# Kernel tuning notes

Hardware: AMD Instinct MI355X
Metric: run time of the kernel (lower is better)

The kernel has to match this reference:

```python
import jax, jax.numpy as jnp
import numpy as np

EMB = 32  # DGM_c.input_dim

def setup_inputs() -> dict:
    key = jax.random.key(0)
    k1, k2, k3 = jax.random.split(key, 3)
    G, n, F = 32, 1024, 128
    N = G * n
    x = jax.random.normal(k1, (N, F), dtype=jnp.float32)
    W = jax.random.normal(k2, (F, EMB), dtype=jnp.float32) / np.sqrt(F)
    temperature = jnp.float32(1.0)   # nn.Parameter init 1.0
    threshold = jnp.float32(0.5)     # nn.Parameter init 0.5
    batch = jnp.repeat(jnp.arange(G, dtype=jnp.int32), n)  # equal-sized graphs
    edge_index = jax.random.randint(k3, (2, 262144), 0, N, dtype=jnp.int32)
    return {"x": x, "W": W, "temperature": temperature, "threshold": threshold,
            "batch": batch, "edge_index": edge_index, "num_graphs": G}


def reference(x, W, temperature, threshold, batch, edge_index, num_graphs):
    # x: [N, F]; equal-sized graphs of n nodes each (batch is sorted, contiguous)
    N = x.shape[0]
    G = num_graphs
    n = N // G

    # embed_f: linear projection to EMB dims (edge structure unused by this embed_f)
    xe = x @ W                                  # [N, EMB]

    # scale<0 branch fires only for the FIRST graph; centroid/scale are detached
    x0 = xe[:n]                                 # graph 0 embedding
    centroid = jax.lax.stop_gradient(jnp.mean(x0, axis=0))             # [EMB]
    scale = jax.lax.stop_gradient(0.9 / jnp.max(jnp.abs(x0 - centroid)))

    xg = ((xe - centroid) * scale).reshape(G, n, EMB)

    # squared pairwise euclidean distances per graph (cdist**2, clamped >= 0)
    sq = jnp.sum(xg * xg, axis=-1)              # [G, n]
    D = jnp.maximum(sq[:, :, None] + sq[:, None, :]
                    - 2.0 * jnp.einsum('gnd,gmd->gnm', xg, xg), 0.0)   # [G, n, n]

    A = jax.nn.sigmoid(temperature * (jnp.abs(threshold) - D))         # [G, n, n]

    # sigmoid > 0 everywhere => dense_to_sparse keeps every entry, row-major,
    # with per-graph node offsets added back.
    edge_weight = A.reshape(-1)                 # [G*n*n]
    ii = jnp.arange(n, dtype=jnp.int32)
    gi = jnp.broadcast_to(ii[:, None], (n, n)).reshape(-1)  # row index
    gj = jnp.broadcast_to(ii[None, :], (n, n)).reshape(-1)  # col index
    off = (jnp.arange(G, dtype=jnp.int32) * n)[:, None]     # [G, 1]
    src = (off + gi[None, :]).reshape(-1)
    dst = (off + gj[None, :]).reshape(-1)
    edge_index_out = jnp.stack([src, dst])      # [2, G*n*n]

    return xe, edge_index_out, edge_weight
```

## Files before the change

### kernel.cpp

```cpp
#include <hip/hip_runtime.h>

#define FDIM 128
#define EMB 32

__global__ __launch_bounds__(256) void k_gemm(const float* __restrict__ x,
                                              const float* __restrict__ Wm,
                                              float* __restrict__ xe) {
    __shared__ float sW[FDIM * EMB];
    const int t = threadIdx.x;
#pragma unroll
    for (int i = 0; i < (FDIM * EMB) / (256 * 4); ++i) {
        int idx = (t + i * 256) * 4;
        *(float4*)(sW + idx) = *(const float4*)(Wm + idx);
    }
    __syncthreads();

    const int r0 = blockIdx.x * 128 + (t >> 3) * 4;
    const int e0 = (t & 7) * 4;

    float acc[4][4];
#pragma unroll
    for (int i = 0; i < 4; ++i)
#pragma unroll
        for (int j = 0; j < 4; ++j) acc[i][j] = 0.f;

    for (int k = 0; k < FDIM; k += 4) {
        float4 w0 = *(const float4*)(sW + (k + 0) * EMB + e0);
        float4 w1 = *(const float4*)(sW + (k + 1) * EMB + e0);
        float4 w2 = *(const float4*)(sW + (k + 2) * EMB + e0);
        float4 w3 = *(const float4*)(sW + (k + 3) * EMB + e0);
#pragma unroll
        for (int rr = 0; rr < 4; ++rr) {
            float4 xq = *(const float4*)(x + (size_t)(r0 + rr) * FDIM + k);
            acc[rr][0] += xq.x * w0.x + xq.y * w1.x + xq.z * w2.x + xq.w * w3.x;
            acc[rr][1] += xq.x * w0.y + xq.y * w1.y + xq.z * w2.y + xq.w * w3.y;
            acc[rr][2] += xq.x * w0.z + xq.y * w1.z + xq.z * w2.z + xq.w * w3.z;
            acc[rr][3] += xq.x * w0.w + xq.y * w1.w + xq.z * w2.w + xq.w * w3.w;
        }
    }

#pragma unroll
    for (int rr = 0; rr < 4; ++rr) {
        const size_t r = (size_t)(r0 + rr);
        float4 o; o.x = acc[rr][0]; o.y = acc[rr][1]; o.z = acc[rr][2]; o.w = acc[rr][3];
        *(float4*)(xe + r * EMB + e0) = o;
    }
}

__global__ __launch_bounds__(256) void k_stats_a(const float* __restrict__ xe,
                                                 float* __restrict__ psum,
                                                 float* __restrict__ pmin,
                                                 float* __restrict__ pmax) {
    __shared__ float rs[256], rmn[256], rmx[256];
    const int t = threadIdx.x;
    const int d = t & 31, rg = t >> 5;
    const int r0 = blockIdx.x * 32;

    float s = 0.f, mn = 3.4e38f, mx = -3.4e38f;
#pragma unroll
    for (int it = 0; it < 4; ++it) {
        float v = xe[(size_t)(r0 + rg + it * 8) * EMB + d];
        s += v;
        mn = fminf(mn, v);
        mx = fmaxf(mx, v);
    }
    rs[t] = s; rmn[t] = mn; rmx[t] = mx;
    __syncthreads();
#pragma unroll
    for (int st = 128; st >= 32; st >>= 1) {
        if (t < st) {
            rs[t] += rs[t + st];
            rmn[t] = fminf(rmn[t], rmn[t + st]);
            rmx[t] = fmaxf(rmx[t], rmx[t + st]);
        }
        __syncthreads();
    }
    if (t < 32) {
        psum[blockIdx.x * 32 + t] = rs[t];
        pmin[blockIdx.x * 32 + t] = rmn[t];
        pmax[blockIdx.x * 32 + t] = rmx[t];
    }
}

__global__ __launch_bounds__(64) void k_stats_b(const float* __restrict__ psum,
                                                const float* __restrict__ pmin,
                                                const float* __restrict__ pmax,
                                                int nb, int n,
                                                float* __restrict__ stats) {
    const int t = threadIdx.x;
    const int d = t & 31;
    float s = 0.f, mn = 3.4e38f, mx = -3.4e38f;
    for (int b = 0; b < nb; ++b) {
        s += psum[b * 32 + d];
        mn = fminf(mn, pmin[b * 32 + d]);
        mx = fmaxf(mx, pmax[b * 32 + d]);
    }
    const float c = s / (float)n;
    float dev = fmaxf(mx - c, c - mn);
#pragma unroll
    for (int off = 16; off >= 1; off >>= 1)
        dev = fmaxf(dev, __shfl_xor(dev, off, 32));
    if (t < 32) stats[t] = c;
    if (t == 0) stats[EMB] = 0.9f / dev;
}

#define LDST 36
__global__ __launch_bounds__(256) void k_edges(const float* __restrict__ xe,
                                               const float* __restrict__ stats,
                                               const float* __restrict__ tptr,
                                               const float* __restrict__ thptr,
                                               float* __restrict__ wts,
                                               float* __restrict__ srcp,
                                               float* __restrict__ dstp,
                                               int n) {
    __shared__ float shA[64 * LDST];
    __shared__ float shB[64 * LDST];
    __shared__ float sqA[64], sqB[64];

    const int g = blockIdx.z;
    const int i0 = blockIdx.y * 64, j0 = blockIdx.x * 64;
    const int t = threadIdx.x;
    const float scale = stats[EMB];

    const float* baseA = xe + ((size_t)g * n + i0) * EMB;
    const float* baseB = xe + ((size_t)g * n + j0) * EMB;

#pragma unroll
    for (int c = 0; c < 2; ++c) {
        int id = t + c * 256;
        int row = id >> 3;
        int dc = (id & 7) * 4;
        int dswz = dc ^ (((row >> 2) & 7) << 2);
        float4 cen = *(const float4*)(stats + dc);
        float4 va = *(const float4*)(baseA + (size_t)row * EMB + dc);
        float4 vb = *(const float4*)(baseB + (size_t)row * EMB + dc);
        va.x = (va.x - cen.x) * scale; va.y = (va.y - cen.y) * scale;
        va.z = (va.z - cen.z) * scale; va.w = (va.w - cen.w) * scale;
        vb.x = (vb.x - cen.x) * scale; vb.y = (vb.y - cen.y) * scale;
        vb.z = (vb.z - cen.z) * scale; vb.w = (vb.w - cen.w) * scale;
        *(float4*)(shA + row * LDST + dc) = va;
        *(float4*)(shB + row * LDST + dswz) = vb;
    }
    __syncthreads();

    if (t < 64) {
        float s = 0.f;
#pragma unroll
        for (int d = 0; d < EMB; d += 4) {
            float4 v = *(const float4*)(shA + t * LDST + d);
            s += v.x * v.x + v.y * v.y + v.z * v.z + v.w * v.w;
        }
        sqA[t] = s;
    } else if (t < 128) {
        int r = t - 64;
        int key = ((r >> 2) & 7) << 2;
        float s = 0.f;
#pragma unroll
        for (int d = 0; d < EMB; d += 4) {
            float4 v = *(const float4*)(shB + r * LDST + (d ^ key));
            s += v.x * v.x + v.y * v.y + v.z * v.z + v.w * v.w;
        }
        sqB[r] = s;
    }
    __syncthreads();

    const int ti = t >> 4, tj = t & 15;
    const int bkey = (tj & 7) << 2;
    float acc[4][4];
#pragma unroll
    for (int i = 0; i < 4; ++i)
#pragma unroll
        for (int j = 0; j < 4; ++j) acc[i][j] = 0.f;

    for (int d = 0; d < EMB; d += 4) {
        float4 a[4], b[4];
#pragma unroll
        for (int u = 0; u < 4; ++u)
            a[u] = *(const float4*)(shA + (ti * 4 + u) * LDST + d);
        const int dsw = d ^ bkey;
#pragma unroll
        for (int v = 0; v < 4; ++v)
            b[v] = *(const float4*)(shB + (tj * 4 + v) * LDST + dsw);
#pragma unroll
        for (int u = 0; u < 4; ++u)
#pragma unroll
            for (int v = 0; v < 4; ++v)
                acc[u][v] += a[u].x * b[v].x + a[u].y * b[v].y +
                             a[u].z * b[v].z + a[u].w * b[v].w;
    }

    const float T = *tptr;
    const float TH = fabsf(*thptr);
    const int gn = g * n;
    const size_t gbase = (size_t)g * n * n;

    const float4 sq4 = *(const float4*)(sqB + tj * 4);
    const float dbase = (float)(gn + j0 + tj * 4);
    float4 dst4; dst4.x = dbase; dst4.y = dbase + 1.f; dst4.z = dbase + 2.f; dst4.w = dbase + 3.f;

#pragma unroll
    for (int u = 0; u < 4; ++u) {
        const int row = i0 + ti * 4 + u;
        const float sa = sqA[ti * 4 + u];
        const size_t off = gbase + (size_t)row * n + j0 + tj * 4;

        float4 w;
        {
            float D0 = fmaxf(sa + sq4.x - 2.f * acc[u][0], 0.f);
            float D1 = fmaxf(sa + sq4.y - 2.f * acc[u][1], 0.f);
            float D2 = fmaxf(sa + sq4.z - 2.f * acc[u][2], 0.f);
            float D3 = fmaxf(sa + sq4.w - 2.f * acc[u][3], 0.f);
            w.x = __builtin_amdgcn_rcpf(1.f + __expf(-(T * (TH - D0))));
            w.y = __builtin_amdgcn_rcpf(1.f + __expf(-(T * (TH - D1))));
            w.z = __builtin_amdgcn_rcpf(1.f + __expf(-(T * (TH - D2))));
            w.w = __builtin_amdgcn_rcpf(1.f + __expf(-(T * (TH - D3))));
        }
        *(float4*)(wts + off) = w;

        const float sv = (float)(gn + row);
        float4 s4; s4.x = sv; s4.y = sv; s4.z = sv; s4.w = sv;
        *(float4*)(srcp + off) = s4;
        *(float4*)(dstp + off) = dst4;
    }
}

extern "C" void kernel_launch(void* const* d_in, const int* in_sizes, int n_in,
                              void* d_out, int out_size, void* d_ws, size_t ws_size,
                              hipStream_t stream) {
    const float* x     = (const float*)d_in[0];
    const float* Wm    = (const float*)d_in[1];
    const float* tptr  = (const float*)d_in[2];
    const float* thptr = (const float*)d_in[3];

    const int N = in_sizes[0] / FDIM;
    const long long rem = (long long)out_size - (long long)N * EMB;
    int G = (rem > 0) ? (int)((3LL * N * N) / rem) : 32;
    if (G <= 0) G = 32;
    const int n = N / G;
    const int nb = n / 32;

    float* out  = (float*)d_out;
    float* xe   = out;
    const long long M = (long long)G * n * n;
    float* srcp = out + (size_t)N * EMB;
    float* dstp = srcp + (size_t)M;
    float* wts  = dstp + (size_t)M;

    float* stats = (float*)d_ws;
    float* psum  = stats + 64;
    float* pmin  = psum + (size_t)nb * 32;
    float* pmax  = pmin + (size_t)nb * 32;

    k_gemm<<<N / 128, 256, 0, stream>>>(x, Wm, xe);
    k_stats_a<<<nb, 256, 0, stream>>>(xe, psum, pmin, pmax);
    k_stats_b<<<1, 64, 0, stream>>>(psum, pmin, pmax, nb, n, stats);
    dim3 ge(n / 64, n / 64, G);
    k_edges<<<ge, 256, 0, stream>>>(xe, stats, tptr, thptr, wts, srcp, dstp, n);
}
```

Measured before the change: 110.7 us.

## Make edge kernel persistent with register-prefetched next tile staging

Replaces the one-block-per-64x64-tile edge kernel with a persistent grid of 1024 blocks, each looping over a contiguous run of tiles. The next tile's embedding rows are loaded into registers while the current tile is computed and stored, then centred, scaled and written to shared memory after a barrier. Row squared norms are computed during staging with a shuffle, and both A and B tiles are now XOR-swizzled. The aim is to hide global load latency and cut per-block launch and prologue cost in a store-bound kernel. In exchange it adds extra barriers per tile and fixes the grid size.

Measured after the change: 114.5 us. 1.04x slower.

```diff
diff --git a/kernel.cpp b/kernel.cpp
--- a/kernel.cpp
+++ b/kernel.cpp
@@ -2,6 +2,7 @@
 
 #define FDIM 128
 #define EMB 32
+#define LDST 36
 
 __global__ __launch_bounds__(256) void k_gemm(const float* __restrict__ x,
                                               const float* __restrict__ Wm,
@@ -60,9 +61,7 @@
 #pragma unroll
     for (int it = 0; it < 4; ++it) {
         float v = xe[(size_t)(r0 + rg + it * 8) * EMB + d];
-        s += v;
-        mn = fminf(mn, v);
-        mx = fmaxf(mx, v);
+        s += v; mn = fminf(mn, v); mx = fmaxf(mx, v);
     }
     rs[t] = s; rmn[t] = mn; rmx[t] = mx;
     __syncthreads();
@@ -104,108 +103,157 @@
     if (t == 0) stats[EMB] = 0.9f / dev;
 }
 
-#define LDST 36
-__global__ __launch_bounds__(256) void k_edges(const float* __restrict__ xe,
-                                               const float* __restrict__ stats,
-                                               const float* __restrict__ tptr,
-                                               const float* __restrict__ thptr,
-                                               float* __restrict__ wts,
-                                               float* __restrict__ srcp,
-                                               float* __restrict__ dstp,
-                                               int n) {
+__global__ __launch_bounds__(256, 4) void k_edges_p(const float* __restrict__ xe,
+                                                    const float* __restrict__ stats,
+                                                    const float* __restrict__ tptr,
+                                                    const float* __restrict__ thptr,
+                                                    float* __restrict__ wts,
+                                                    float* __restrict__ srcp,
+                                                    float* __restrict__ dstp,
+                                                    int n, int ntiles, int tpb) {
     __shared__ float shA[64 * LDST];
     __shared__ float shB[64 * LDST];
     __shared__ float sqA[64], sqB[64];
 
-    const int g = blockIdx.z;
-    const int i0 = blockIdx.y * 64, j0 = blockIdx.x * 64;
     const int t = threadIdx.x;
+    const int t0 = blockIdx.x * tpb;
+    int cnt = ntiles - t0;
+    if (cnt <= 0) return;
+    if (cnt > tpb) cnt = tpb;
+
+    const int tprow = n >> 6;
+    const int tpg = tprow * tprow;
+
     const float scale = stats[EMB];
-
-    const float* baseA = xe + ((size_t)g * n + i0) * EMB;
-    const float* baseB = xe + ((size_t)g * n + j0) * EMB;
-
-#pragma unroll
-    for (int c = 0; c < 2; ++c) {
-        int id = t + c * 256;
-        int row = id >> 3;
-        int dc = (id & 7) * 4;
-        int dswz = dc ^ (((row >> 2) & 7) << 2);
-        float4 cen = *(const float4*)(stats + dc);
-        float4 va = *(const float4*)(baseA + (size_t)row * EMB + dc);
-        float4 vb = *(const float4*)(baseB + (size_t)row * EMB + dc);
-        va.x = (va.x - cen.x) * scale; va.y = (va.y - cen.y) * scale;
-        va.z = (va.z - cen.z) * scale; va.w = (va.w - cen.w) * scale;
-        vb.x = (vb.x - cen.x) * scale; vb.y = (vb.y - cen.y) * scale;
-        vb.z = (vb.z - cen.z) * scale; vb.w = (vb.w - cen.w) * scale;
-        *(float4*)(shA + row * LDST + dc) = va;
-        *(float4*)(shB + row * LDST + dswz) = vb;
-    }
-    __syncthreads();
-
-    if (t < 64) {
-        float s = 0.f;
-#pragma unroll
-        for (int d = 0; d < EMB; d += 4) {
-            float4 v = *(const float4*)(shA + t * LDST + d);
-            s += v.x * v.x + v.y * v.y + v.z * v.z + v.w * v.w;
-        }
-        sqA[t] = s;
-    } else if (t < 128) {
-        int r = t - 64;
-        int key = ((r >> 2) & 7) << 2;
-        float s = 0.f;
-#pragma unroll
-        for (int d = 0; d < EMB; d += 4) {
-            float4 v = *(const float4*)(shB + r * LDST + (d ^ key));
-            s += v.x * v.x + v.y * v.y + v.z * v.z + v.w * v.w;
-        }
-        sqB[r] = s;
-    }
-    __syncthreads();
-
-    const int ti = t >> 4, tj = t & 15;
-    const int bkey = (tj & 7) << 2;
-    float acc[4][4];
-#pragma unroll
-    for (int i = 0; i < 4; ++i)
-#pragma unroll
-        for (int j = 0; j < 4; ++j) acc[i][j] = 0.f;
-
-    for (int d = 0; d < EMB; d += 4) {
-        float4 a[4], b[4];
-#pragma unroll
-        for (int u = 0; u < 4; ++u)
-            a[u] = *(const float4*)(shA + (ti * 4 + u) * LDST + d);
-        const int dsw = d ^ bkey;
-#pragma unroll
-        for (int v = 0; v < 4; ++v)
-            b[v] = *(const float4*)(shB + (tj * 4 + v) * LDST + dsw);
-#pragma unroll
-        for (int u = 0; u < 4; ++u)
-#pragma unroll
-            for (int v = 0; v < 4; ++v)
-                acc[u][v] += a[u].x * b[v].x + a[u].y * b[v].y +
-                             a[u].z * b[v].z + a[u].w * b[v].w;
-    }
-
     const float T = *tptr;
     const float TH = fabsf(*thptr);
-    const int gn = g * n;
-    const size_t gbase = (size_t)g * n * n;
-
-    const float4 sq4 = *(const float4*)(sqB + tj * 4);
-    const float dbase = (float)(gn + j0 + tj * 4);
-    float4 dst4; dst4.x = dbase; dst4.y = dbase + 1.f; dst4.z = dbase + 2.f; dst4.w = dbase + 3.f;
-
-#pragma unroll
-    for (int u = 0; u < 4; ++u) {
-        const int row = i0 + ti * 4 + u;
-        const float sa = sqA[ti * 4 + u];
-        const size_t off = gbase + (size_t)row * n + j0 + tj * 4;
-
-        float4 w;
-        {
+
+    const int sideB = (t >= 128);
+    const int tid2 = t & 127;
+    const int rid = tid2 >> 1;
+    const int half = tid2 & 1;
+    const int skey = ((rid >> 2) & 7) << 2;
+    const int cbase = half * 16;
+
+    const float4 cen0 = *(const float4*)(stats + cbase + 0);
+    const float4 cen1 = *(const float4*)(stats + cbase + 4);
+    const float4 cen2 = *(const float4*)(stats + cbase + 8);
+    const float4 cen3 = *(const float4*)(stats + cbase + 12);
+
+    const int ti = t >> 4, tj = t & 15;
+    const int akey = (ti & 7) << 2;
+    const int bkey = (tj & 7) << 2;
+
+#define COORDS(tt, g_, i0_, j0_)                                              \
+    {                                                                         \
+        g_ = (tt) / tpg;                                                      \
+        int r_ = (tt) - g_ * tpg;                                             \
+        i0_ = (r_ / tprow) * 64;                                              \
+        j0_ = (r_ - (r_ / tprow) * tprow) * 64;                               \
+    }
+
+#define LOADT(g_, i0_, j0_, l0, l1, l2, l3)                                   \
+    {                                                                         \
+        const int row_ = (sideB ? (j0_) : (i0_)) + rid;                       \
+        const float* p_ = xe + ((size_t)((g_)*n + row_)) * EMB + cbase;       \
+        l0 = *(const float4*)(p_ + 0);                                        \
+        l1 = *(const float4*)(p_ + 4);                                        \
+        l2 = *(const float4*)(p_ + 8);                                        \
+        l3 = *(const float4*)(p_ + 12);                                       \
+    }
+
+#define STAGE(l0, l1, l2, l3)                                                 \
+    {                                                                         \
+        l0.x = (l0.x - cen0.x) * scale; l0.y = (l0.y - cen0.y) * scale;       \
+        l0.z = (l0.z - cen0.z) * scale; l0.w = (l0.w - cen0.w) * scale;       \
+        l1.x = (l1.x - cen1.x) * scale; l1.y = (l1.y - cen1.y) * scale;       \
+        l1.z = (l1.z - cen1.z) * scale; l1.w = (l1.w - cen1.w) * scale;       \
+        l2.x = (l2.x - cen2.x) * scale; l2.y = (l2.y - cen2.y) * scale;       \
+        l2.z = (l2.z - cen2.z) * scale; l2.w = (l2.w - cen2.w) * scale;       \
+        l3.x = (l3.x - cen3.x) * scale; l3.y = (l3.y - cen3.y) * scale;       \
+        l3.z = (l3.z - cen3.z) * scale; l3.w = (l3.w - cen3.w) * scale;       \
+        float ps_ = l0.x*l0.x + l0.y*l0.y + l0.z*l0.z + l0.w*l0.w             \
+                  + l1.x*l1.x + l1.y*l1.y + l1.z*l1.z + l1.w*l1.w             \
+                  + l2.x*l2.x + l2.y*l2.y + l2.z*l2.z + l2.w*l2.w             \
+                  + l3.x*l3.x + l3.y*l3.y + l3.z*l3.z + l3.w*l3.w;            \
+        float tot_ = ps_ + __shfl_xor(ps_, 1);                                \
+        float* sh_ = sideB ? shB : shA;                                       \
+        *(float4*)(sh_ + rid * LDST + ((cbase + 0) ^ skey))  = l0;            \
+        *(float4*)(sh_ + rid * LDST + ((cbase + 4) ^ skey))  = l1;            \
+        *(float4*)(sh_ + rid * LDST + ((cbase + 8) ^ skey))  = l2;            \
+        *(float4*)(sh_ + rid * LDST + ((cbase + 12) ^ skey)) = l3;            \
+        if (half == 0) { if (sideB) sqB[rid] = tot_; else sqA[rid] = tot_; }  \
+    }
+
+#define RAWBAR()                                                              \
+    {                                                                         \
+        __builtin_amdgcn_sched_barrier(0);                                    \
+        __builtin_amdgcn_s_barrier();                                         \
+        __builtin_amdgcn_sched_barrier(0);                                    \
+    }
+
+    {
+        int g, i0, j0;
+        COORDS(t0, g, i0, j0);
+        float4 l0, l1, l2, l3;
+        LOADT(g, i0, j0, l0, l1, l2, l3);
+        STAGE(l0, l1, l2, l3);
+    }
+    asm volatile("s_waitcnt lgkmcnt(0)" ::: "memory");
+    RAWBAR();
+
+    for (int k = 0; k < cnt; ++k) {
+        const int tt = t0 + k;
+        int g, i0, j0;
+        COORDS(tt, g, i0, j0);
+
+        const int have = (k + 1 < cnt);
+        float4 l0, l1, l2, l3;
+        if (have) {
+            int g2, i02, j02;
+            COORDS(tt + 1, g2, i02, j02);
+            LOADT(g2, i02, j02, l0, l1, l2, l3);
+        }
+
+        float acc[4][4];
+#pragma unroll
+        for (int i = 0; i < 4; ++i)
+#pragma unroll
+            for (int j = 0; j < 4; ++j) acc[i][j] = 0.f;
+
+#pragma unroll
+        for (int d = 0; d < EMB; d += 4) {
+            float4 a[4], b[4];
+            const int da = d ^ akey;
+            const int db = d ^ bkey;
+#pragma unroll
+            for (int u = 0; u < 4; ++u)
+                a[u] = *(const float4*)(shA + (ti * 4 + u) * LDST + da);
+#pragma unroll
+            for (int v = 0; v < 4; ++v)
+                b[v] = *(const float4*)(shB + (tj * 4 + v) * LDST + db);
+#pragma unroll
+            for (int u = 0; u < 4; ++u)
+#pragma unroll
+                for (int v = 0; v < 4; ++v)
+                    acc[u][v] += a[u].x * b[v].x + a[u].y * b[v].y +
+                                 a[u].z * b[v].z + a[u].w * b[v].w;
+        }
+
+        const int gn = g * n;
+        const size_t gbase = (size_t)g * n * n;
+        const float4 sq4 = *(const float4*)(sqB + tj * 4);
+        const float dbase = (float)(gn + j0 + tj * 4);
+        float4 dst4; dst4.x = dbase; dst4.y = dbase + 1.f;
+        dst4.z = dbase + 2.f; dst4.w = dbase + 3.f;
+
+#pragma unroll
+        for (int u = 0; u < 4; ++u) {
+            const int row = i0 + ti * 4 + u;
+            const float sa = sqA[ti * 4 + u];
+            const size_t off = gbase + (size_t)row * n + j0 + tj * 4;
+
+            float4 w;
             float D0 = fmaxf(sa + sq4.x - 2.f * acc[u][0], 0.f);
             float D1 = fmaxf(sa + sq4.y - 2.f * acc[u][1], 0.f);
             float D2 = fmaxf(sa + sq4.z - 2.f * acc[u][2], 0.f);
@@ -214,14 +262,26 @@
             w.y = __builtin_amdgcn_rcpf(1.f + __expf(-(T * (TH - D1))));
             w.z = __builtin_amdgcn_rcpf(1.f + __expf(-(T * (TH - D2))));
             w.w = __builtin_amdgcn_rcpf(1.f + __expf(-(T * (TH - D3))));
-        }
-        *(float4*)(wts + off) = w;
-
-        const float sv = (float)(gn + row);
-        float4 s4; s4.x = sv; s4.y = sv; s4.z = sv; s4.w = sv;
-        *(float4*)(srcp + off) = s4;
-        *(float4*)(dstp + off) = dst4;
-    }
+            *(float4*)(wts + off) = w;
+
+            const float sv = (float)(gn + row);
+            float4 s4; s4.x = sv; s4.y = sv; s4.z = sv; s4.w = sv;
+            *(float4*)(srcp + off) = s4;
+            *(float4*)(dstp + off) = dst4;
+        }
+
+        RAWBAR();
+
+        if (have) {
+            STAGE(l0, l1, l2, l3);
+        }
+        asm volatile("s_waitcnt lgkmcnt(0)" ::: "memory");
+        RAWBAR();
+    }
+#undef COORDS
+#undef LOADT
+#undef STAGE
+#undef RAWBAR
 }
 
 extern "C" void kernel_launch(void* const* d_in, const int* in_sizes, int n_in,
@@ -254,6 +314,11 @@
     k_gemm<<<N / 128, 256, 0, stream>>>(x, Wm, xe);
     k_stats_a<<<nb, 256, 0, stream>>>(xe, psum, pmin, pmax);
     k_stats_b<<<1, 64, 0, stream>>>(psum, pmin, pmax, nb, n, stats);
-    dim3 ge(n / 64, n / 64, G);
-    k_edges<<<ge, 256, 0, stream>>>(xe, stats, tptr, thptr, wts, srcp, dstp, n);
-}
+
+    const int tprow = n / 64;
+    const int ntiles = tprow * tprow * G;
+    const int nblocks = 1024;
+    const int tpb = (ntiles + nblocks - 1) / nblocks;
+    k_edges_p<<<nblocks, 256, 0, stream>>>(xe, stats, tptr, thptr,
+                                           wts, srcp, dstp, n, ntiles, tpb);
+}
```

## Make edge kernel persistent per row strip with double-buffered column tiles

Applied to the files above, without the earlier changes.

Replaces the 3D tile grid with one block per 64-row strip per graph. Each block loops over all column tiles, prefetching the next B tile into registers and double-buffering it in LDS. Row squared norms are now computed with warp shuffles during the load, and A is swizzled too. This removes redundant A loads and per-block setup, but greatly reduces the number of blocks and waves available to hide store latency.

Measured after the change: 137.4 us. 1.24x slower.

```diff
diff --git a/kernel.cpp b/kernel.cpp
--- a/kernel.cpp
+++ b/kernel.cpp
@@ -60,9 +60,7 @@
 #pragma unroll
     for (int it = 0; it < 4; ++it) {
         float v = xe[(size_t)(r0 + rg + it * 8) * EMB + d];
-        s += v;
-        mn = fminf(mn, v);
-        mx = fmaxf(mx, v);
+        s += v; mn = fminf(mn, v); mx = fmaxf(mx, v);
     }
     rs[t] = s; rmn[t] = mn; rmx[t] = mx;
     __syncthreads();
@@ -104,123 +102,162 @@
     if (t == 0) stats[EMB] = 0.9f / dev;
 }
 
-#define LDST 36
-__global__ __launch_bounds__(256) void k_edges(const float* __restrict__ xe,
-                                               const float* __restrict__ stats,
-                                               const float* __restrict__ tptr,
-                                               const float* __restrict__ thptr,
-                                               float* __restrict__ wts,
-                                               float* __restrict__ srcp,
-                                               float* __restrict__ dstp,
-                                               int n) {
-    __shared__ float shA[64 * LDST];
-    __shared__ float shB[64 * LDST];
-    __shared__ float sqA[64], sqB[64];
-
-    const int g = blockIdx.z;
-    const int i0 = blockIdx.y * 64, j0 = blockIdx.x * 64;
+#define KEY(r) ((((r) >> 2) & 7) << 2)
+__global__ __launch_bounds__(256) void k_edges_s(const float* __restrict__ xe,
+                                                 const float* __restrict__ stats,
+                                                 const float* __restrict__ tptr,
+                                                 const float* __restrict__ thptr,
+                                                 float* __restrict__ wts,
+                                                 float* __restrict__ srcp,
+                                                 float* __restrict__ dstp,
+                                                 int n) {
+    __shared__ float shA[64 * 32];
+    __shared__ float shB[2][64 * 32];
+    __shared__ float sqA[64];
+    __shared__ float sqB[2][64];
+
+    const int g = blockIdx.y;
+    const int i0 = blockIdx.x * 64;
     const int t = threadIdx.x;
     const float scale = stats[EMB];
 
-    const float* baseA = xe + ((size_t)g * n + i0) * EMB;
-    const float* baseB = xe + ((size_t)g * n + j0) * EMB;
-
-#pragma unroll
-    for (int c = 0; c < 2; ++c) {
-        int id = t + c * 256;
-        int row = id >> 3;
-        int dc = (id & 7) * 4;
-        int dswz = dc ^ (((row >> 2) & 7) << 2);
-        float4 cen = *(const float4*)(stats + dc);
-        float4 va = *(const float4*)(baseA + (size_t)row * EMB + dc);
-        float4 vb = *(const float4*)(baseB + (size_t)row * EMB + dc);
-        va.x = (va.x - cen.x) * scale; va.y = (va.y - cen.y) * scale;
-        va.z = (va.z - cen.z) * scale; va.w = (va.w - cen.w) * scale;
-        vb.x = (vb.x - cen.x) * scale; vb.y = (vb.y - cen.y) * scale;
-        vb.z = (vb.z - cen.z) * scale; vb.w = (vb.w - cen.w) * scale;
-        *(float4*)(shA + row * LDST + dc) = va;
-        *(float4*)(shB + row * LDST + dswz) = vb;
+    const int srow = t >> 2;
+    const int sdc = (t & 3) * 8;
+    const int skey = KEY(srow);
+    const float4 cenL = *(const float4*)(stats + sdc);
+    const float4 cenH = *(const float4*)(stats + sdc + 4);
+    const float* gbaseXe = xe + (size_t)g * n * EMB;
+
+    {
+        const float* p = gbaseXe + (size_t)(i0 + srow) * EMB + sdc;
+        float4 vL = *(const float4*)(p);
+        float4 vH = *(const float4*)(p + 4);
+        vL.x = (vL.x - cenL.x) * scale; vL.y = (vL.y - cenL.y) * scale;
+        vL.z = (vL.z - cenL.z) * scale; vL.w = (vL.w - cenL.w) * scale;
+        vH.x = (vH.x - cenH.x) * scale; vH.y = (vH.y - cenH.y) * scale;
+        vH.z = (vH.z - cenH.z) * scale; vH.w = (vH.w - cenH.w) * scale;
+        *(float4*)(shA + srow * 32 + (sdc ^ skey)) = vL;
+        *(float4*)(shA + srow * 32 + ((sdc + 4) ^ skey)) = vH;
+        float ps = vL.x*vL.x + vL.y*vL.y + vL.z*vL.z + vL.w*vL.w
+                 + vH.x*vH.x + vH.y*vH.y + vH.z*vH.z + vH.w*vH.w;
+        ps += __shfl_xor(ps, 1);
+        ps += __shfl_xor(ps, 2);
+        if ((t & 3) == 0) sqA[srow] = ps;
+    }
+
+    {
+        const float* p = gbaseXe + (size_t)srow * EMB + sdc;
+        float4 vL = *(const float4*)(p);
+        float4 vH = *(const float4*)(p + 4);
+        vL.x = (vL.x - cenL.x) * scale; vL.y = (vL.y - cenL.y) * scale;
+        vL.z = (vL.z - cenL.z) * scale; vL.w = (vL.w - cenL.w) * scale;
+        vH.x = (vH.x - cenH.x) * scale; vH.y = (vH.y - cenH.y) * scale;
+        vH.z = (vH.z - cenH.z) * scale; vH.w = (vH.w - cenH.w) * scale;
+        *(float4*)(shB[0] + srow * 32 + (sdc ^ skey)) = vL;
+        *(float4*)(shB[0] + srow * 32 + ((sdc + 4) ^ skey)) = vH;
+        float ps = vL.x*vL.x + vL.y*vL.y + vL.z*vL.z + vL.w*vL.w
+                 + vH.x*vH.x + vH.y*vH.y + vH.z*vH.z + vH.w*vH.w;
+        ps += __shfl_xor(ps, 1);
+        ps += __shfl_xor(ps, 2);
+        if ((t & 3) == 0) sqB[0][srow] = ps;
     }
     __syncthreads();
-
-    if (t < 64) {
-        float s = 0.f;
-#pragma unroll
-        for (int d = 0; d < EMB; d += 4) {
-            float4 v = *(const float4*)(shA + t * LDST + d);
-            s += v.x * v.x + v.y * v.y + v.z * v.z + v.w * v.w;
-        }
-        sqA[t] = s;
-    } else if (t < 128) {
-        int r = t - 64;
-        int key = ((r >> 2) & 7) << 2;
-        float s = 0.f;
-#pragma unroll
-        for (int d = 0; d < EMB; d += 4) {
-            float4 v = *(const float4*)(shB + r * LDST + (d ^ key));
-            s += v.x * v.x + v.y * v.y + v.z * v.z + v.w * v.w;
-        }
-        sqB[r] = s;
-    }
-    __syncthreads();
-
-    const int ti = t >> 4, tj = t & 15;
-    const int bkey = (tj & 7) << 2;
-    float acc[4][4];
-#pragma unroll
-    for (int i = 0; i < 4; ++i)
-#pragma unroll
-        for (int j = 0; j < 4; ++j) acc[i][j] = 0.f;
-
-    for (int d = 0; d < EMB; d += 4) {
-        float4 a[4], b[4];
-#pragma unroll
-        for (int u = 0; u < 4; ++u)
-            a[u] = *(const float4*)(shA + (ti * 4 + u) * LDST + d);
-        const int dsw = d ^ bkey;
-#pragma unroll
-        for (int v = 0; v < 4; ++v)
-            b[v] = *(const float4*)(shB + (tj * 4 + v) * LDST + dsw);
-#pragma unroll
-        for (int u = 0; u < 4; ++u)
-#pragma unroll
-            for (int v = 0; v < 4; ++v)
-                acc[u][v] += a[u].x * b[v].x + a[u].y * b[v].y +
-                             a[u].z * b[v].z + a[u].w * b[v].w;
-    }
 
     const float T = *tptr;
     const float TH = fabsf(*thptr);
     const int gn = g * n;
     const size_t gbase = (size_t)g * n * n;
 
-    const float4 sq4 = *(const float4*)(sqB + tj * 4);
-    const float dbase = (float)(gn + j0 + tj * 4);
-    float4 dst4; dst4.x = dbase; dst4.y = dbase + 1.f; dst4.z = dbase + 2.f; dst4.w = dbase + 3.f;
-
-#pragma unroll
-    for (int u = 0; u < 4; ++u) {
-        const int row = i0 + ti * 4 + u;
-        const float sa = sqA[ti * 4 + u];
-        const size_t off = gbase + (size_t)row * n + j0 + tj * 4;
-
-        float4 w;
-        {
-            float D0 = fmaxf(sa + sq4.x - 2.f * acc[u][0], 0.f);
-            float D1 = fmaxf(sa + sq4.y - 2.f * acc[u][1], 0.f);
-            float D2 = fmaxf(sa + sq4.z - 2.f * acc[u][2], 0.f);
-            float D3 = fmaxf(sa + sq4.w - 2.f * acc[u][3], 0.f);
-            w.x = __builtin_amdgcn_rcpf(1.f + __expf(-(T * (TH - D0))));
-            w.y = __builtin_amdgcn_rcpf(1.f + __expf(-(T * (TH - D1))));
-            w.z = __builtin_amdgcn_rcpf(1.f + __expf(-(T * (TH - D2))));
-            w.w = __builtin_amdgcn_rcpf(1.f + __expf(-(T * (TH - D3))));
-        }
-        *(float4*)(wts + off) = w;
-
-        const float sv = (float)(gn + row);
-        float4 s4; s4.x = sv; s4.y = sv; s4.z = sv; s4.w = sv;
-        *(float4*)(srcp + off) = s4;
-        *(float4*)(dstp + off) = dst4;
+    const int ti = t >> 4, tj = t & 15;
+    const int akey = (ti & 7) << 2;
+    const int bkey = (tj & 7) << 2;
+    const int ntiles = n >> 6;
+
+    for (int jt = 0; jt < ntiles; ++jt) {
+        const int cur = jt & 1;
+        const int j0 = jt * 64;
+
+        float4 nL, nH;
+        const int have = (jt + 1 < ntiles);
+        if (have) {
+            const float* p = gbaseXe + (size_t)((jt + 1) * 64 + srow) * EMB + sdc;
+            nL = *(const float4*)(p);
+            nH = *(const float4*)(p + 4);
+        }
+
+        float acc[4][4];
+#pragma unroll
+        for (int i = 0; i < 4; ++i)
+#pragma unroll
+            for (int j = 0; j < 4; ++j) acc[i][j] = 0.f;
+
+        const float* sB = shB[cur];
+#pragma unroll
+        for (int d = 0; d < EMB; d += 4) {
+            float4 a[4], b[4];
+            const int dsa = d ^ akey;
+            const int dsb = d ^ bkey;
+#pragma unroll
+            for (int u = 0; u < 4; ++u)
+                a[u] = *(const float4*)(shA + (ti * 4 + u) * 32 + dsa);
+#pragma unroll
+            for (int v = 0; v < 4; ++v)
+                b[v] = *(const float4*)(sB + (tj * 4 + v) * 32 + dsb);
+#pragma unroll
+            for (int u = 0; u < 4; ++u)
+#pragma unroll
+                for (int v = 0; v < 4; ++v)
+                    acc[u][v] += a[u].x * b[v].x + a[u].y * b[v].y +
+                                 a[u].z * b[v].z + a[u].w * b[v].w;
+        }
+
+        const float4 sq4 = *(const float4*)(&sqB[cur][tj * 4]);
+        const float dbase = (float)(gn + j0 + tj * 4);
+        float4 dst4; dst4.x = dbase; dst4.y = dbase + 1.f;
+        dst4.z = dbase + 2.f; dst4.w = dbase + 3.f;
+
+#pragma unroll
+        for (int u = 0; u < 4; ++u) {
+            const int row = i0 + ti * 4 + u;
+            const float sa = sqA[ti * 4 + u];
+            const size_t off = gbase + (size_t)row * n + j0 + tj * 4;
+
+            float4 w;
+            {
+                float D0 = fmaxf(sa + sq4.x - 2.f * acc[u][0], 0.f);
+                float D1 = fmaxf(sa + sq4.y - 2.f * acc[u][1], 0.f);
+                float D2 = fmaxf(sa + sq4.z - 2.f * acc[u][2], 0.f);
+                float D3 = fmaxf(sa + sq4.w - 2.f * acc[u][3], 0.f);
+                w.x = __builtin_amdgcn_rcpf(1.f + __expf(-(T * (TH - D0))));
+                w.y = __builtin_amdgcn_rcpf(1.f + __expf(-(T * (TH - D1))));
+                w.z = __builtin_amdgcn_rcpf(1.f + __expf(-(T * (TH - D2))));
+                w.w = __builtin_amdgcn_rcpf(1.f + __expf(-(T * (TH - D3))));
+            }
+            *(float4*)(wts + off) = w;
+
+            const float sv = (float)(gn + row);
+            float4 s4; s4.x = sv; s4.y = sv; s4.z = sv; s4.w = sv;
+            *(float4*)(srcp + off) = s4;
+            *(float4*)(dstp + off) = dst4;
+        }
+
+        __syncthreads();
+
+        if (have) {
+            nL.x = (nL.x - cenL.x) * scale; nL.y = (nL.y - cenL.y) * scale;
+            nL.z = (nL.z - cenL.z) * scale; nL.w = (nL.w - cenL.w) * scale;
+            nH.x = (nH.x - cenH.x) * scale; nH.y = (nH.y - cenH.y) * scale;
+            nH.z = (nH.z - cenH.z) * scale; nH.w = (nH.w - cenH.w) * scale;
+            float* dstB = shB[1 - cur];
+            *(float4*)(dstB + srow * 32 + (sdc ^ skey)) = nL;
+            *(float4*)(dstB + srow * 32 + ((sdc + 4) ^ skey)) = nH;
+            float ps = nL.x*nL.x + nL.y*nL.y + nL.z*nL.z + nL.w*nL.w
+                     + nH.x*nH.x + nH.y*nH.y + nH.z*nH.z + nH.w*nH.w;
+            ps += __shfl_xor(ps, 1);
+            ps += __shfl_xor(ps, 2);
+            if ((t & 3) == 0) sqB[1 - cur][srow] = ps;
+        }
+        __syncthreads();
     }
 }
 
@@ -254,6 +291,6 @@
     k_gemm<<<N / 128, 256, 0, stream>>>(x, Wm, xe);
     k_stats_a<<<nb, 256, 0, stream>>>(xe, psum, pmin, pmax);
     k_stats_b<<<1, 64, 0, stream>>>(psum, pmin, pmax, nb, n, stats);
-    dim3 ge(n / 64, n / 64, G);
-    k_edges<<<ge, 256, 0, stream>>>(xe, stats, tptr, thptr, wts, srcp, dstp, n);
-}
+    dim3 ge(n / 64, G);
+    k_edges_s<<<ge, 256, 0, stream>>>(xe, stats, tptr, thptr, wts, srcp, dstp, n);
+}
```
